# Performance work log

Hardware: AMD Instinct MI355X
Metric: run time of the kernel (lower is better)

Reference implementation:

```python
import jax, jax.numpy as jnp
import numpy as np
from jax import lax

V, E, H, K, PAD = 30000, 128, 256, 32, 0
B, T = 128, 256


def setup_inputs() -> dict:
    key = jax.random.key(0)
    ks = jax.random.split(key, 16)

    def n(k, shape, s=0.1):
        return jax.random.normal(k, shape, jnp.float32) * s

    embed = n(ks[0], (V, E)).at[PAD].set(0.0)  # padding_idx row zeroed
    wih_f = n(ks[1], (4 * H, E)); whh_f = n(ks[2], (4 * H, H))
    bih_f = n(ks[3], (4 * H,));   bhh_f = n(ks[4], (4 * H,))
    wih_b = n(ks[5], (4 * H, E)); whh_b = n(ks[6], (4 * H, H))
    bih_b = n(ks[7], (4 * H,));   bhh_b = n(ks[8], (4 * H,))
    w_lin = n(ks[9], (K, 2 * H)); b_lin = n(ks[10], (K,))
    start_t = n(ks[11], (K,)); end_t = n(ks[12], (K,)); trans = n(ks[13], (K, K))
    tokens = jax.random.randint(ks[14], (B, T), 0, V)
    lengths = jax.random.randint(ks[15], (B,), 1, T + 1)
    mask = jnp.arange(T)[None, :] < lengths[:, None]  # mask[:,0] always True
    return {"input": tokens, "mask": mask, "embed": embed,
            "wih_f": wih_f, "whh_f": whh_f, "bih_f": bih_f, "bhh_f": bhh_f,
            "wih_b": wih_b, "whh_b": whh_b, "bih_b": bih_b, "bhh_b": bhh_b,
            "w_lin": w_lin, "b_lin": b_lin,
            "start_t": start_t, "end_t": end_t, "trans": trans}


def _lstm(x, wih, whh, bih, bhh, reverse):
    # x: [B,T,E]; torch gate order i,f,g,o
    Bq, _, _ = x.shape
    Hh = whh.shape[1]
    pre = jnp.einsum('bte,ge->btg', x, wih) + bih + bhh  # [B,T,4H]
    pre = jnp.swapaxes(pre, 0, 1)  # [T,B,4H]

    def step(carry, p):
        h, c = carry
        g = p + h @ whh.T
        i, f, gg, o = jnp.split(g, 4, axis=-1)
        c = jax.nn.sigmoid(f) * c + jax.nn.sigmoid(i) * jnp.tanh(gg)
        h = jax.nn.sigmoid(o) * jnp.tanh(c)
        return (h, c), h

    init = (jnp.zeros((Bq, Hh), x.dtype), jnp.zeros((Bq, Hh), x.dtype))
    _, hs = lax.scan(step, init, pre, reverse=reverse)
    return jnp.swapaxes(hs, 0, 1)  # [B,T,H]


def _emissions(input, embed, wih_f, whh_f, bih_f, bhh_f, wih_b, whh_b, bih_b, bhh_b, w_lin, b_lin):
    x = embed[input]                               # [B,T,E]
    hf = _lstm(x, wih_f, whh_f, bih_f, bhh_f, False)
    hb = _lstm(x, wih_b, whh_b, bih_b, bhh_b, True)
    return jnp.concatenate([hf, hb], -1) @ w_lin.T + b_lin  # [B,T,K]


def _viterbi(em, mask, start_t, end_t, trans):
    Bq, Tq, Kq = em.shape
    score = start_t + em[:, 0]                     # [B,K]
    em_t = jnp.swapaxes(em, 0, 1)[1:]              # [T-1,B,K]
    m_t = jnp.swapaxes(mask, 0, 1)[1:]             # [T-1,B]

    def step(score, em_m):
        emt, m = em_m
        cand = score[:, :, None] + trans[None] + emt[:, None, :]  # [B,K,K]
        best = cand.max(axis=1)
        idx = jnp.argmax(cand, axis=1)             # [B,K] best prev tag
        return jnp.where(m[:, None], best, score), idx

    score, hist = lax.scan(step, score, (em_t, m_t))  # hist [T-1,B,K]
    last = jnp.argmax(score + end_t, axis=-1)      # [B] tag at last valid pos

    def back(idx, hist_m):
        h, m = hist_m
        prev = jnp.take_along_axis(h, idx[:, None], axis=1)[:, 0]
        new = jnp.where(m, prev, idx)
        return new, new

    _, tags_head = lax.scan(back, last, (hist, m_t), reverse=True)  # [T-1,B]
    tags = jnp.concatenate([tags_head, last[None]], axis=0)         # [T,B]
    tags = jnp.swapaxes(tags, 0, 1)
    return jnp.where(mask, tags, 0).astype(jnp.int32)


def reference(input, mask, embed, wih_f, whh_f, bih_f, bhh_f, wih_b, whh_b, bih_b, bhh_b, w_lin, b_lin, start_t, end_t, trans):
    em = _emissions(input, embed, wih_f, whh_f, bih_f, bhh_f,
                    wih_b, whh_b, bih_b, bhh_b, w_lin, b_lin)
    return _viterbi(em, mask, start_t, end_t, trans)
```

## Files before the change

### kernel.cpp

```cpp
#include <hip/hip_runtime.h>
#include <hip/hip_bf16.h>

#define B_ 128
#define T_ 256
#define E_ 128
#define H_ 256
#define K_ 32
#define G4H 1024

__device__ __forceinline__ float sigf(float z) { return 1.0f / (1.0f + expf(-z)); }

__global__ void k_lengths(const unsigned* __restrict__ maskw, int* __restrict__ lengths) {
  __shared__ int flagBad;
  __shared__ int flagOdd;
  int tid = threadIdx.x;
  if (tid == 0) { flagBad = 0; flagOdd = 0; }
  __syncthreads();
  int bad = 0, odd = 0;
  for (int i = tid; i < (B_ * T_) / 4; i += 256) {
    unsigned v = maskw[i];
    if (v > 1u) bad = 1;
    if ((i & 1) && v) odd = 1;
  }
  if (bad) atomicOr(&flagBad, 1);
  if (odd) atomicOr(&flagOdd, 1);
  __syncthreads();
  int mode = flagBad ? 0 : (flagOdd ? 1 : 2);
  for (int b = tid; b < B_; b += 256) {
    int cnt = 0;
    if (mode == 0) {
      const unsigned char* mb = (const unsigned char*)maskw;
      for (int t = 0; t < T_; ++t) cnt += (mb[b * T_ + t] != 0);
    } else if (mode == 1) {
      for (int t = 0; t < T_; ++t) cnt += (maskw[b * T_ + t] != 0);
    } else {
      for (int t = 0; t < T_; ++t) cnt += (maskw[(size_t)(b * T_ + t) * 2] != 0);
    }
    if (cnt < 1) cnt = 1;
    lengths[b] = cnt;
  }
}

__global__ void k_packw4(const float* __restrict__ wih_f, const float* __restrict__ whh_f,
                         const float* __restrict__ wih_b, const float* __restrict__ whh_b,
                         float* __restrict__ wpk) {
  int e = blockIdx.x * 256 + threadIdx.x;
  if (e >= 786432) return;
  int p = e & 3;
  int g = (e >> 2) & 63;
  int rest = e >> 8;
  int k4 = rest % 96;
  int dus = rest / 96;
  int us = dus & 15, d = dus >> 4;
  int brow = (g >> 4) * 256 + us * 16 + (g & 15);
  int k = k4 * 4 + p;
  const float* wih = d ? wih_b : wih_f;
  const float* whh = d ? whh_b : whh_f;
  wpk[e] = (k < E_) ? wih[brow * E_ + k] : whh[brow * H_ + (k - E_)];
}

__global__ void k_bias(const float* __restrict__ bih_f, const float* __restrict__ bhh_f,
                       const float* __restrict__ bih_b, const float* __restrict__ bhh_b,
                       float* __restrict__ bias) {
  int e = blockIdx.x * 256 + threadIdx.x;
  if (e >= 2 * G4H) return;
  int d = e >> 10, j = e & 1023;
  bias[e] = d ? (bih_b[j] + bhh_b[j]) : (bih_f[j] + bhh_f[j]);
}

__global__ void k_gather(const int* __restrict__ tokens, const float* __restrict__ embed,
                         float* __restrict__ x) {
  int idx = blockIdx.x * 256 + threadIdx.x;
  int p = idx >> 5, e4 = idx & 31;
  int tok = tokens[p];
  ((float4*)x)[(size_t)p * 32 + e4] = ((const float4*)embed)[(size_t)tok * 32 + e4];
}

__global__ void k_zero(int* __restrict__ flags) {
  int i = blockIdx.x * 256 + threadIdx.x;
  if (i < 16384) flags[i] = 0;
}

__global__ __launch_bounds__(512) void k_lstm4(const float* __restrict__ x,
    const float* __restrict__ wpk, const float* __restrict__ bias,
    float* __restrict__ hf, float* __restrict__ hb,
    float* __restrict__ hx, int* __restrict__ flags) {
  const int wg = blockIdx.x;
  const int us = wg & 15;
  const int rb = (wg >> 4) & 7;
  const int d  = wg >> 7;
  const int b0 = rb * 16;
  const int tid = threadIdx.x;
  __shared__ float4 wL[96 * 64];
  __shared__ float4 vL[96 * 16];
  __shared__ float  gbuf2[2 * 64 * 17];

  {
    const float4* wsrc = (const float4*)(wpk + (size_t)(d * 16 + us) * 24576);
    for (int i = tid; i < 6144; i += 512) wL[i] = wsrc[i];
  }
  const int r2 = tid & 7;
  const int gg = (tid >> 3) & 31;
  const int kc = tid >> 8;
  const int g0 = 2 * gg, g1 = g0 + 1;
  const int uu = tid & 15, rr = (tid >> 4) & 15;
  const int sk4 = tid >> 4, sr = tid & 15;
  float b_i = 0.f, b_f = 0.f, b_g = 0.f, b_o = 0.f;
  if (tid < 256) {
    b_i = bias[d * G4H + 0 * 256 + us * 16 + uu];
    b_f = bias[d * G4H + 1 * 256 + us * 16 + uu];
    b_g = bias[d * G4H + 2 * 256 + us * 16 + uu];
    b_o = bias[d * G4H + 3 * 256 + us * 16 + uu];
  }
  float creg = 0.f;
  float4 xr;
  {
    int t0 = d ? (T_ - 1) : 0;
    xr = *(const float4*)(x + ((size_t)(b0 + sr) * T_ + t0) * E_ + sk4 * 4);
  }
  float* __restrict__ hout = d ? hb : hf;
  float* __restrict__ hxg = hx + (size_t)(d * 8 + rb) * 8192;
  int* __restrict__ flagg = flags + (d * 8 + rb) * 1024;
  __syncthreads();

  for (int s = 0; s < T_; ++s) {
    const int t = d ? (T_ - 1 - s) : s;
    if (s > 0 && tid < 16) {
      int* fp = flagg + tid * 64;
      while (__hip_atomic_load(fp, __ATOMIC_RELAXED, __HIP_MEMORY_SCOPE_AGENT) < s) {}
    }
    __syncthreads();
    vL[sk4 * 16 + sr] = xr;
    if (s == 0) {
#pragma unroll
      for (int it = 0; it < 8; ++it) {
        int i = it * 512 + tid;
        ((float*)vL)[(32 + (i >> 6)) * 64 + (i & 15) * 4 + ((i >> 4) & 3)] = 0.f;
      }
    } else {
      const float* hsrc = hxg + (size_t)(s & 1) * 4096;
#pragma unroll
      for (int it = 0; it < 8; ++it) {
        int i = it * 512 + tid;
        float hv = __hip_atomic_load(hsrc + i, __ATOMIC_RELAXED, __HIP_MEMORY_SCOPE_AGENT);
        ((float*)vL)[(32 + (i >> 6)) * 64 + (i & 15) * 4 + ((i >> 4) & 3)] = hv;
      }
    }
    __syncthreads();
    if (s + 1 < T_) {
      int tn = d ? (T_ - 2 - s) : (s + 1);
      xr = *(const float4*)(x + ((size_t)(b0 + sr) * T_ + tn) * E_ + sk4 * 4);
    }
    float a00 = 0.f, a01 = 0.f, a10 = 0.f, a11 = 0.f;
    {
      const float4* wp = wL + kc * 48 * 64;
      const float4* vp = vL + kc * 48 * 16;
#pragma unroll 4
      for (int k4 = 0; k4 < 48; ++k4) {
        float4 w0 = wp[k4 * 64 + g0];
        float4 w1 = wp[k4 * 64 + g1];
        float4 v0 = vp[k4 * 16 + 2 * r2];
        float4 v1 = vp[k4 * 16 + 2 * r2 + 1];
        a00 += w0.x * v0.x + w0.y * v0.y + w0.z * v0.z + w0.w * v0.w;
        a01 += w0.x * v1.x + w0.y * v1.y + w0.z * v1.z + w0.w * v1.w;
        a10 += w1.x * v0.x + w1.y * v0.y + w1.z * v0.z + w1.w * v0.w;
        a11 += w1.x * v1.x + w1.y * v1.y + w1.z * v1.z + w1.w * v1.w;
      }
    }
    gbuf2[kc * 1088 + g0 * 17 + 2 * r2]     = a00;
    gbuf2[kc * 1088 + g0 * 17 + 2 * r2 + 1] = a01;
    gbuf2[kc * 1088 + g1 * 17 + 2 * r2]     = a10;
    gbuf2[kc * 1088 + g1 * 17 + 2 * r2 + 1] = a11;
    __syncthreads();
    if (tid < 256) {
      float ig = gbuf2[uu * 17 + rr]        + gbuf2[1088 + uu * 17 + rr]        + b_i;
      float fg = gbuf2[(16 + uu) * 17 + rr] + gbuf2[1088 + (16 + uu) * 17 + rr] + b_f;
      float gv = gbuf2[(32 + uu) * 17 + rr] + gbuf2[1088 + (32 + uu) * 17 + rr] + b_g;
      float og = gbuf2[(48 + uu) * 17 + rr] + gbuf2[1088 + (48 + uu) * 17 + rr] + b_o;
      creg = sigf(fg) * creg + sigf(ig) * tanhf(gv);
      float hn = sigf(og) * tanhf(creg);
      hout[((size_t)(b0 + rr) * T_ + t) * H_ + us * 16 + uu] = hn;
      __hip_atomic_store(hxg + (size_t)((s + 1) & 1) * 4096 + (us * 16 + uu) * 16 + rr, hn,
                         __ATOMIC_RELAXED, __HIP_MEMORY_SCOPE_AGENT);
    }
    asm volatile("s_waitcnt vmcnt(0)" ::: "memory");
    __syncthreads();
    if (tid == 0)
      __hip_atomic_store(flagg + us * 64, s + 1, __ATOMIC_RELEASE, __HIP_MEMORY_SCOPE_AGENT);
  }
}

__global__ __launch_bounds__(256) void k_emis(const float* __restrict__ hf, const float* __restrict__ hb,
    const float* __restrict__ w_lin, const float* __restrict__ b_lin, float* __restrict__ em) {
  __shared__ float hsl[8][512];
  __shared__ float red[8][8][K_];
  const int tid = threadIdx.x;
  const int pos0 = blockIdx.x * 8;
  for (int it = 0; it < 4; ++it) {
    int idx = it * 256 + tid;
    int rr = idx >> 7, c4 = idx & 127;
    const float* src = (c4 < 64) ? (hf + ((size_t)(pos0 + rr)) * H_ + (c4 * 4))
                                 : (hb + ((size_t)(pos0 + rr)) * H_ + ((c4 - 64) * 4));
    float4 v = *(const float4*)src;
    *(float4*)&hsl[rr][c4 * 4] = v;
  }
  __syncthreads();
  const int k = tid & 31, jc = tid >> 5;
  float wreg[64];
#pragma unroll
  for (int i4 = 0; i4 < 16; ++i4) {
    float4 w = *(const float4*)(w_lin + (size_t)k * 512 + jc * 64 + i4 * 4);
    wreg[i4 * 4 + 0] = w.x; wreg[i4 * 4 + 1] = w.y; wreg[i4 * 4 + 2] = w.z; wreg[i4 * 4 + 3] = w.w;
  }
  float acc[8];
  for (int rr = 0; rr < 8; ++rr) {
    float a = 0.f;
#pragma unroll
    for (int i4 = 0; i4 < 16; ++i4) {
      float4 h = *(const float4*)&hsl[rr][jc * 64 + i4 * 4];
      a += wreg[i4 * 4 + 0] * h.x + wreg[i4 * 4 + 1] * h.y + wreg[i4 * 4 + 2] * h.z + wreg[i4 * 4 + 3] * h.w;
    }
    acc[rr] = a;
  }
  for (int rr2 = 0; rr2 < 8; ++rr2) red[rr2][jc][k] = acc[rr2];
  __syncthreads();
  {
    int rr = tid >> 5, kk = tid & 31;
    float s = b_lin[kk];
#pragma unroll
    for (int j = 0; j < 8; ++j) s += red[rr][j][kk];
    em[((size_t)(pos0 + rr)) * K_ + kk] = s;
  }
}

__global__ __launch_bounds__(64) void k_viterbi(const float* __restrict__ em,
    const int* __restrict__ lengths, const float* __restrict__ start_t,
    const float* __restrict__ end_t, const float* __restrict__ trans,
    int* __restrict__ out) {
  const int b = blockIdx.x;
  const int lane = threadIdx.x;
  __shared__ unsigned char hist[T_ - 1][K_];
  __shared__ float sl[K_];
  const int len = lengths[b];
  float tc[K_];
  float score = 0.f;
  if (lane < K_) {
#pragma unroll
    for (int i = 0; i < K_; ++i) tc[i] = trans[i * K_ + lane];
    score = start_t[lane] + em[((size_t)b * T_) * K_ + lane];
  }
  for (int t = 1; t < T_; ++t) {
    float emk = 0.f;
    if (lane < K_) {
      emk = em[((size_t)b * T_ + t) * K_ + lane];
      sl[lane] = score;
    }
    __syncthreads();
    if (lane < K_) {
      float best = sl[0] + tc[0]; int bi = 0;
#pragma unroll
      for (int i = 1; i < K_; ++i) {
        float c = sl[i] + tc[i];
        if (c > best) { best = c; bi = i; }
      }
      hist[t - 1][lane] = (unsigned char)bi;
      if (t < len) score = best + emk;
    }
    __syncthreads();
  }
  if (lane < K_) sl[lane] = score + end_t[lane];
  __syncthreads();
  int* outb = out + (size_t)b * T_;
  for (int t = lane; t < T_; t += 64)
    if (t >= len) outb[t] = 0;
  if (lane == 0) {
    float best = sl[0]; int cur = 0;
    for (int k2 = 1; k2 < K_; ++k2)
      if (sl[k2] > best) { best = sl[k2]; cur = k2; }
    outb[len - 1] = cur;
    for (int t = len - 2; t >= 0; --t) { cur = hist[t][cur]; outb[t] = cur; }
  }
}

extern "C" void kernel_launch(void* const* d_in, const int* in_sizes, int n_in,
                              void* d_out, int out_size, void* d_ws, size_t ws_size,
                              hipStream_t stream) {
  const int* tokens   = (const int*)d_in[0];
  const unsigned* maskw = (const unsigned*)d_in[1];
  const float* embed  = (const float*)d_in[2];
  const float* wih_f  = (const float*)d_in[3];
  const float* whh_f  = (const float*)d_in[4];
  const float* bih_f  = (const float*)d_in[5];
  const float* bhh_f  = (const float*)d_in[6];
  const float* wih_b  = (const float*)d_in[7];
  const float* whh_b  = (const float*)d_in[8];
  const float* bih_b  = (const float*)d_in[9];
  const float* bhh_b  = (const float*)d_in[10];
  const float* w_lin  = (const float*)d_in[11];
  const float* b_lin  = (const float*)d_in[12];
  const float* start_t = (const float*)d_in[13];
  const float* end_t  = (const float*)d_in[14];
  const float* trans  = (const float*)d_in[15];
  int* out = (int*)d_out;
  (void)in_sizes; (void)n_in; (void)out_size; (void)ws_size;

  char* ws = (char*)d_ws;
  size_t off = 0;
  auto alloc = [&](size_t bytes) { size_t o = off; off = (off + bytes + 255) & ~(size_t)255; return o; };
  int*   lengths = (int*)(ws + alloc((size_t)B_ * 4));
  float* wpk     = (float*)(ws + alloc((size_t)786432 * 4));
  float* bias    = (float*)(ws + alloc((size_t)2 * G4H * 4));
  float* x       = (float*)(ws + alloc((size_t)B_ * T_ * E_ * 4));
  float* hf      = (float*)(ws + alloc((size_t)B_ * T_ * H_ * 4));
  float* hb      = (float*)(ws + alloc((size_t)B_ * T_ * H_ * 4));
  float* em      = (float*)(ws + alloc((size_t)B_ * T_ * K_ * 4));
  float* hx      = (float*)(ws + alloc((size_t)16 * 8192 * 4));
  int*   flags   = (int*)(ws + alloc((size_t)16384 * 4));

  k_lengths<<<dim3(1), dim3(256), 0, stream>>>(maskw, lengths);
  k_packw4<<<dim3(3072), dim3(256), 0, stream>>>(wih_f, whh_f, wih_b, whh_b, wpk);
  k_bias<<<dim3(8), dim3(256), 0, stream>>>(bih_f, bhh_f, bih_b, bhh_b, bias);
  k_gather<<<dim3((B_ * T_ * E_ / 4) / 256), dim3(256), 0, stream>>>(tokens, embed, x);
  k_zero<<<dim3(64), dim3(256), 0, stream>>>(flags);
  k_lstm4<<<dim3(256), dim3(512), 0, stream>>>(x, wpk, bias, hf, hb, hx, flags);
  k_emis<<<dim3(B_ * T_ / 8), dim3(256), 0, stream>>>(hf, hb, w_lin, b_lin, em);
  k_viterbi<<<dim3(B_), dim3(64), 0, stream>>>(em, lengths, start_t, end_t, trans, out);
}
```

Measured before the change: 3.180 ms.

## Overlap input-projection matmul with cross-block hidden-state wait in LSTM

Splits the packed LSTM weights into separate input and recurrent blocks so each step can compute the x·Wih contribution before spinning on the inter-workgroup flags. The recurrent part runs only after the hidden state from other workgroups arrives. The global h output store and the next x prefetch move after the flag release, which takes them off the critical path. This adds an extra __syncthreads per step and splits the pack kernel in two.

Result: faster. 3.058 ms (-3.8%).

```diff
diff --git a/kernel.cpp b/kernel.cpp
--- a/kernel.cpp
+++ b/kernel.cpp
@@ -41,22 +41,32 @@
   }
 }
 
-__global__ void k_packw4(const float* __restrict__ wih_f, const float* __restrict__ whh_f,
-                         const float* __restrict__ wih_b, const float* __restrict__ whh_b,
-                         float* __restrict__ wpk) {
+__global__ void k_packw3A(const float* __restrict__ wih_f, const float* __restrict__ wih_b,
+                          float* __restrict__ wpkA) {
   int e = blockIdx.x * 256 + threadIdx.x;
-  if (e >= 786432) return;
-  int p = e & 3;
-  int g = (e >> 2) & 63;
-  int rest = e >> 8;
-  int k4 = rest % 96;
-  int dus = rest / 96;
-  int us = dus & 15, d = dus >> 4;
+  if (e >= 262144) return;
+  int p  = e & 3;
+  int g  = (e >> 2) & 63;
+  int k4 = (e >> 8) & 31;
+  int us = (e >> 13) & 15;
+  int d  = (e >> 17) & 1;
   int brow = (g >> 4) * 256 + us * 16 + (g & 15);
-  int k = k4 * 4 + p;
   const float* wih = d ? wih_b : wih_f;
+  wpkA[e] = wih[brow * E_ + k4 * 4 + p];
+}
+
+__global__ void k_packw3B(const float* __restrict__ whh_f, const float* __restrict__ whh_b,
+                          float* __restrict__ wpkB) {
+  int e = blockIdx.x * 256 + threadIdx.x;
+  if (e >= 524288) return;
+  int p  = e & 3;
+  int g  = (e >> 2) & 63;
+  int k4 = (e >> 8) & 63;
+  int us = (e >> 14) & 15;
+  int d  = (e >> 18) & 1;
+  int brow = (g >> 4) * 256 + us * 16 + (g & 15);
   const float* whh = d ? whh_b : whh_f;
-  wpk[e] = (k < E_) ? wih[brow * E_ + k] : whh[brow * H_ + (k - E_)];
+  wpkB[e] = whh[brow * H_ + k4 * 4 + p];
 }
 
 __global__ void k_bias(const float* __restrict__ bih_f, const float* __restrict__ bhh_f,
@@ -81,8 +91,9 @@
   if (i < 16384) flags[i] = 0;
 }
 
-__global__ __launch_bounds__(512) void k_lstm4(const float* __restrict__ x,
-    const float* __restrict__ wpk, const float* __restrict__ bias,
+__global__ __launch_bounds__(512) void k_lstm5(const float* __restrict__ x,
+    const float* __restrict__ wpkA, const float* __restrict__ wpkB,
+    const float* __restrict__ bias,
     float* __restrict__ hf, float* __restrict__ hb,
     float* __restrict__ hx, int* __restrict__ flags) {
   const int wg = blockIdx.x;
@@ -91,13 +102,17 @@
   const int d  = wg >> 7;
   const int b0 = rb * 16;
   const int tid = threadIdx.x;
-  __shared__ float4 wL[96 * 64];
-  __shared__ float4 vL[96 * 16];
+  __shared__ float4 wA[32 * 64];
+  __shared__ float4 wB[64 * 64];
+  __shared__ float4 vx[32 * 16];
+  __shared__ float4 vLh[64 * 16];
   __shared__ float  gbuf2[2 * 64 * 17];
 
   {
-    const float4* wsrc = (const float4*)(wpk + (size_t)(d * 16 + us) * 24576);
-    for (int i = tid; i < 6144; i += 512) wL[i] = wsrc[i];
+    const float4* srcA = (const float4*)(wpkA + (size_t)(d * 16 + us) * 8192);
+    for (int i = tid; i < 2048; i += 512) wA[i] = srcA[i];
+    const float4* srcB = (const float4*)(wpkB + (size_t)(d * 16 + us) * 16384);
+    for (int i = tid; i < 4096; i += 512) wB[i] = srcB[i];
   }
   const int r2 = tid & 7;
   const int gg = (tid >> 3) & 31;
@@ -112,12 +127,17 @@
     b_g = bias[d * G4H + 2 * 256 + us * 16 + uu];
     b_o = bias[d * G4H + 3 * 256 + us * 16 + uu];
   }
-  float creg = 0.f;
+  float creg = 0.f, hn = 0.f;
   float4 xr;
   {
     int t0 = d ? (T_ - 1) : 0;
     xr = *(const float4*)(x + ((size_t)(b0 + sr) * T_ + t0) * E_ + sk4 * 4);
   }
+  vx[sk4 * 16 + sr] = xr;
+  {
+    int t1 = d ? (T_ - 2) : 1;
+    xr = *(const float4*)(x + ((size_t)(b0 + sr) * T_ + t1) * E_ + sk4 * 4);
+  }
   float* __restrict__ hout = d ? hb : hf;
   float* __restrict__ hxg = hx + (size_t)(d * 8 + rb) * 8192;
   int* __restrict__ flagg = flags + (d * 8 + rb) * 1024;
@@ -125,38 +145,12 @@
 
   for (int s = 0; s < T_; ++s) {
     const int t = d ? (T_ - 1 - s) : s;
-    if (s > 0 && tid < 16) {
-      int* fp = flagg + tid * 64;
-      while (__hip_atomic_load(fp, __ATOMIC_RELAXED, __HIP_MEMORY_SCOPE_AGENT) < s) {}
-    }
-    __syncthreads();
-    vL[sk4 * 16 + sr] = xr;
-    if (s == 0) {
-#pragma unroll
-      for (int it = 0; it < 8; ++it) {
-        int i = it * 512 + tid;
-        ((float*)vL)[(32 + (i >> 6)) * 64 + (i & 15) * 4 + ((i >> 4) & 3)] = 0.f;
-      }
-    } else {
-      const float* hsrc = hxg + (size_t)(s & 1) * 4096;
-#pragma unroll
-      for (int it = 0; it < 8; ++it) {
-        int i = it * 512 + tid;
-        float hv = __hip_atomic_load(hsrc + i, __ATOMIC_RELAXED, __HIP_MEMORY_SCOPE_AGENT);
-        ((float*)vL)[(32 + (i >> 6)) * 64 + (i & 15) * 4 + ((i >> 4) & 3)] = hv;
-      }
-    }
-    __syncthreads();
-    if (s + 1 < T_) {
-      int tn = d ? (T_ - 2 - s) : (s + 1);
-      xr = *(const float4*)(x + ((size_t)(b0 + sr) * T_ + tn) * E_ + sk4 * 4);
-    }
     float a00 = 0.f, a01 = 0.f, a10 = 0.f, a11 = 0.f;
     {
-      const float4* wp = wL + kc * 48 * 64;
-      const float4* vp = vL + kc * 48 * 16;
+      const float4* wp = wA + kc * 1024;
+      const float4* vp = vx + kc * 256;
 #pragma unroll 4
-      for (int k4 = 0; k4 < 48; ++k4) {
+      for (int k4 = 0; k4 < 16; ++k4) {
         float4 w0 = wp[k4 * 64 + g0];
         float4 w1 = wp[k4 * 64 + g1];
         float4 v0 = vp[k4 * 16 + 2 * r2];
@@ -167,6 +161,42 @@
         a11 += w1.x * v1.x + w1.y * v1.y + w1.z * v1.z + w1.w * v1.w;
       }
     }
+    if (s > 0 && tid < 16) {
+      int* fp = flagg + tid * 64;
+      while (__hip_atomic_load(fp, __ATOMIC_RELAXED, __HIP_MEMORY_SCOPE_AGENT) < s) {}
+    }
+    __syncthreads();
+    if (s == 0) {
+#pragma unroll
+      for (int it = 0; it < 8; ++it) {
+        int i = it * 512 + tid;
+        ((float*)vLh)[(i >> 6) * 64 + (i & 15) * 4 + ((i >> 4) & 3)] = 0.f;
+      }
+    } else {
+      const float* hsrc = hxg + (size_t)(s & 1) * 4096;
+#pragma unroll
+      for (int it = 0; it < 8; ++it) {
+        int i = it * 512 + tid;
+        float hv = __hip_atomic_load(hsrc + i, __ATOMIC_RELAXED, __HIP_MEMORY_SCOPE_AGENT);
+        ((float*)vLh)[(i >> 6) * 64 + (i & 15) * 4 + ((i >> 4) & 3)] = hv;
+      }
+    }
+    __syncthreads();
+    {
+      const float4* wp = wB + kc * 2048;
+      const float4* vp = vLh + kc * 512;
+#pragma unroll 4
+      for (int k4 = 0; k4 < 32; ++k4) {
+        float4 w0 = wp[k4 * 64 + g0];
+        float4 w1 = wp[k4 * 64 + g1];
+        float4 v0 = vp[k4 * 16 + 2 * r2];
+        float4 v1 = vp[k4 * 16 + 2 * r2 + 1];
+        a00 += w0.x * v0.x + w0.y * v0.y + w0.z * v0.z + w0.w * v0.w;
+        a01 += w0.x * v1.x + w0.y * v1.y + w0.z * v1.z + w0.w * v1.w;
+        a10 += w1.x * v0.x + w1.y * v0.y + w1.z * v0.z + w1.w * v0.w;
+        a11 += w1.x * v1.x + w1.y * v1.y + w1.z * v1.z + w1.w * v1.w;
+      }
+    }
     gbuf2[kc * 1088 + g0 * 17 + 2 * r2]     = a00;
     gbuf2[kc * 1088 + g0 * 17 + 2 * r2 + 1] = a01;
     gbuf2[kc * 1088 + g1 * 17 + 2 * r2]     = a10;
@@ -178,8 +208,7 @@
       float gv = gbuf2[(32 + uu) * 17 + rr] + gbuf2[1088 + (32 + uu) * 17 + rr] + b_g;
       float og = gbuf2[(48 + uu) * 17 + rr] + gbuf2[1088 + (48 + uu) * 17 + rr] + b_o;
       creg = sigf(fg) * creg + sigf(ig) * tanhf(gv);
-      float hn = sigf(og) * tanhf(creg);
-      hout[((size_t)(b0 + rr) * T_ + t) * H_ + us * 16 + uu] = hn;
+      hn = sigf(og) * tanhf(creg);
       __hip_atomic_store(hxg + (size_t)((s + 1) & 1) * 4096 + (us * 16 + uu) * 16 + rr, hn,
                          __ATOMIC_RELAXED, __HIP_MEMORY_SCOPE_AGENT);
     }
@@ -187,6 +216,16 @@
     __syncthreads();
     if (tid == 0)
       __hip_atomic_store(flagg + us * 64, s + 1, __ATOMIC_RELEASE, __HIP_MEMORY_SCOPE_AGENT);
+    if (tid < 256)
+      hout[((size_t)(b0 + rr) * T_ + t) * H_ + us * 16 + uu] = hn;
+    if (s + 1 < T_) {
+      vx[sk4 * 16 + sr] = xr;
+      if (s + 2 < T_) {
+        int tn = d ? (T_ - 3 - s) : (s + 2);
+        xr = *(const float4*)(x + ((size_t)(b0 + sr) * T_ + tn) * E_ + sk4 * 4);
+      }
+    }
+    __syncthreads();
   }
 }
 
@@ -308,7 +347,8 @@
   size_t off = 0;
   auto alloc = [&](size_t bytes) { size_t o = off; off = (off + bytes + 255) & ~(size_t)255; return o; };
   int*   lengths = (int*)(ws + alloc((size_t)B_ * 4));
-  float* wpk     = (float*)(ws + alloc((size_t)786432 * 4));
+  float* wpkA    = (float*)(ws + alloc((size_t)262144 * 4));
+  float* wpkB    = (float*)(ws + alloc((size_t)524288 * 4));
   float* bias    = (float*)(ws + alloc((size_t)2 * G4H * 4));
   float* x       = (float*)(ws + alloc((size_t)B_ * T_ * E_ * 4));
   float* hf      = (float*)(ws + alloc((size_t)B_ * T_ * H_ * 4));
@@ -318,11 +358,12 @@
   int*   flags   = (int*)(ws + alloc((size_t)16384 * 4));
 
   k_lengths<<<dim3(1), dim3(256), 0, stream>>>(maskw, lengths);
-  k_packw4<<<dim3(3072), dim3(256), 0, stream>>>(wih_f, whh_f, wih_b, whh_b, wpk);
+  k_packw3A<<<dim3(1024), dim3(256), 0, stream>>>(wih_f, wih_b, wpkA);
+  k_packw3B<<<dim3(2048), dim3(256), 0, stream>>>(whh_f, whh_b, wpkB);
   k_bias<<<dim3(8), dim3(256), 0, stream>>>(bih_f, bhh_f, bih_b, bhh_b, bias);
   k_gather<<<dim3((B_ * T_ * E_ / 4) / 256), dim3(256), 0, stream>>>(tokens, embed, x);
   k_zero<<<dim3(64), dim3(256), 0, stream>>>(flags);
-  k_lstm4<<<dim3(256), dim3(512), 0, stream>>>(x, wpk, bias, hf, hb, hx, flags);
+  k_lstm5<<<dim3(256), dim3(512), 0, stream>>>(x, wpkA, wpkB, bias, hf, hb, hx, flags);
   k_emis<<<dim3(B_ * T_ / 8), dim3(256), 0, stream>>>(hf, hb, w_lin, b_lin, em);
   k_viterbi<<<dim3(B_), dim3(64), 0, stream>>>(em, lengths, start_t, end_t, trans, out);
 }
```

## Overlap input-projection with flag wait and retile LSTM step as 4x4 register blocks

Applied to the files above, without the earlier changes.

The recurrent LSTM kernel now computes the x·Wih part of the gates before spinning on the cross-workgroup flags, so that work is hidden behind the wait for the previous hidden state. The per-thread tile becomes 4 gates × 4 rows over 8 K-slices, with a matching weight repack and an 8-way reduction buffer. The hout global store and the next x prefetch move after the flag release to shorten the critical path. The cost is an extra barrier per step, a larger shared-memory reduction buffer, and more registers held per thread.

Measured after the change: 3.020 ms. 1.05x faster.

```diff
diff --git a/kernel.cpp b/kernel.cpp
--- a/kernel.cpp
+++ b/kernel.cpp
@@ -9,6 +9,9 @@
 #define G4H 1024
 
 __device__ __forceinline__ float sigf(float z) { return 1.0f / (1.0f + expf(-z)); }
+__device__ __forceinline__ float dot4(float4 a, float4 b) {
+  return a.x * b.x + a.y * b.y + a.z * b.z + a.w * b.w;
+}
 
 __global__ void k_lengths(const unsigned* __restrict__ maskw, int* __restrict__ lengths) {
   __shared__ int flagBad;
@@ -41,22 +44,33 @@
   }
 }
 
-__global__ void k_packw4(const float* __restrict__ wih_f, const float* __restrict__ whh_f,
+__global__ void k_packw6(const float* __restrict__ wih_f, const float* __restrict__ whh_f,
                          const float* __restrict__ wih_b, const float* __restrict__ whh_b,
                          float* __restrict__ wpk) {
   int e = blockIdx.x * 256 + threadIdx.x;
   if (e >= 786432) return;
   int p = e & 3;
-  int g = (e >> 2) & 63;
-  int rest = e >> 8;
-  int k4 = rest % 96;
-  int dus = rest / 96;
-  int us = dus & 15, d = dus >> 4;
-  int brow = (g >> 4) * 256 + us * 16 + (g & 15);
-  int k = k4 * 4 + p;
+  int j = (e >> 2) & 63;
+  int gi = j >> 4, gq = j & 15;
+  int g = gq * 4 + gi;
+  int iter = (e >> 8) % 12;
+  int q = (e >> 8) / 12;
+  int slice = q & 7;
+  int us = (q >> 3) & 15;
+  int d = q >> 7;
+  int ty = g >> 4, u = g & 15;
+  int brow = ty * 256 + us * 16 + u;
   const float* wih = d ? wih_b : wih_f;
   const float* whh = d ? whh_b : whh_f;
-  wpk[e] = (k < E_) ? wih[brow * E_ + k] : whh[brow * H_ + (k - E_)];
+  float v;
+  if (iter < 4) {
+    int k4 = slice * 4 + iter;
+    v = wih[brow * E_ + k4 * 4 + p];
+  } else {
+    int k4 = slice * 8 + (iter - 4);
+    v = whh[brow * H_ + k4 * 4 + p];
+  }
+  wpk[e] = v;
 }
 
 __global__ void k_bias(const float* __restrict__ bih_f, const float* __restrict__ bhh_f,
@@ -81,7 +95,7 @@
   if (i < 16384) flags[i] = 0;
 }
 
-__global__ __launch_bounds__(512) void k_lstm4(const float* __restrict__ x,
+__global__ __launch_bounds__(512) void k_lstm6(const float* __restrict__ x,
     const float* __restrict__ wpk, const float* __restrict__ bias,
     float* __restrict__ hf, float* __restrict__ hb,
     float* __restrict__ hx, int* __restrict__ flags) {
@@ -91,18 +105,18 @@
   const int d  = wg >> 7;
   const int b0 = rb * 16;
   const int tid = threadIdx.x;
-  __shared__ float4 wL[96 * 64];
-  __shared__ float4 vL[96 * 16];
-  __shared__ float  gbuf2[2 * 64 * 17];
+  __shared__ float4 wL[8 * 12 * 64];
+  __shared__ float4 vx[32 * 16];
+  __shared__ float4 vLh[64 * 16];
+  __shared__ float  gbuf[8 * 64 * 17];
 
   {
     const float4* wsrc = (const float4*)(wpk + (size_t)(d * 16 + us) * 24576);
     for (int i = tid; i < 6144; i += 512) wL[i] = wsrc[i];
   }
-  const int r2 = tid & 7;
-  const int gg = (tid >> 3) & 31;
-  const int kc = tid >> 8;
-  const int g0 = 2 * gg, g1 = g0 + 1;
+  const int slice = tid >> 6;
+  const int gq = (tid >> 2) & 15;
+  const int rq = tid & 3;
   const int uu = tid & 15, rr = (tid >> 4) & 15;
   const int sk4 = tid >> 4, sr = tid & 15;
   float b_i = 0.f, b_f = 0.f, b_g = 0.f, b_o = 0.f;
@@ -112,30 +126,50 @@
     b_g = bias[d * G4H + 2 * 256 + us * 16 + uu];
     b_o = bias[d * G4H + 3 * 256 + us * 16 + uu];
   }
-  float creg = 0.f;
+  float creg = 0.f, hn = 0.f;
   float4 xr;
   {
     int t0 = d ? (T_ - 1) : 0;
     xr = *(const float4*)(x + ((size_t)(b0 + sr) * T_ + t0) * E_ + sk4 * 4);
   }
+  vx[sk4 * 16 + sr] = xr;
+  {
+    int t1 = d ? (T_ - 2) : 1;
+    xr = *(const float4*)(x + ((size_t)(b0 + sr) * T_ + t1) * E_ + sk4 * 4);
+  }
   float* __restrict__ hout = d ? hb : hf;
   float* __restrict__ hxg = hx + (size_t)(d * 8 + rb) * 8192;
   int* __restrict__ flagg = flags + (d * 8 + rb) * 1024;
+  const float4* wbase = wL + slice * 12 * 64;
   __syncthreads();
 
   for (int s = 0; s < T_; ++s) {
     const int t = d ? (T_ - 1 - s) : s;
+    float a00 = 0.f, a01 = 0.f, a02 = 0.f, a03 = 0.f;
+    float a10 = 0.f, a11 = 0.f, a12 = 0.f, a13 = 0.f;
+    float a20 = 0.f, a21 = 0.f, a22 = 0.f, a23 = 0.f;
+    float a30 = 0.f, a31 = 0.f, a32 = 0.f, a33 = 0.f;
+#pragma unroll
+    for (int it = 0; it < 4; ++it) {
+      const float4* wp = wbase + it * 64;
+      const float4* vp = vx + (slice * 4 + it) * 16 + rq * 4;
+      float4 w0 = wp[gq], w1 = wp[16 + gq], w2 = wp[32 + gq], w3 = wp[48 + gq];
+      float4 v0 = vp[0], v1 = vp[1], v2 = vp[2], v3 = vp[3];
+      a00 += dot4(w0, v0); a01 += dot4(w0, v1); a02 += dot4(w0, v2); a03 += dot4(w0, v3);
+      a10 += dot4(w1, v0); a11 += dot4(w1, v1); a12 += dot4(w1, v2); a13 += dot4(w1, v3);
+      a20 += dot4(w2, v0); a21 += dot4(w2, v1); a22 += dot4(w2, v2); a23 += dot4(w2, v3);
+      a30 += dot4(w3, v0); a31 += dot4(w3, v1); a32 += dot4(w3, v2); a33 += dot4(w3, v3);
+    }
     if (s > 0 && tid < 16) {
       int* fp = flagg + tid * 64;
       while (__hip_atomic_load(fp, __ATOMIC_RELAXED, __HIP_MEMORY_SCOPE_AGENT) < s) {}
     }
     __syncthreads();
-    vL[sk4 * 16 + sr] = xr;
     if (s == 0) {
 #pragma unroll
       for (int it = 0; it < 8; ++it) {
         int i = it * 512 + tid;
-        ((float*)vL)[(32 + (i >> 6)) * 64 + (i & 15) * 4 + ((i >> 4) & 3)] = 0.f;
+        ((float*)vLh)[(i >> 6) * 64 + (i & 15) * 4 + ((i >> 4) & 3)] = 0.f;
       }
     } else {
       const float* hsrc = hxg + (size_t)(s & 1) * 4096;
@@ -143,43 +177,42 @@
       for (int it = 0; it < 8; ++it) {
         int i = it * 512 + tid;
         float hv = __hip_atomic_load(hsrc + i, __ATOMIC_RELAXED, __HIP_MEMORY_SCOPE_AGENT);
-        ((float*)vL)[(32 + (i >> 6)) * 64 + (i & 15) * 4 + ((i >> 4) & 3)] = hv;
-      }
-    }
-    __syncthreads();
-    if (s + 1 < T_) {
-      int tn = d ? (T_ - 2 - s) : (s + 1);
-      xr = *(const float4*)(x + ((size_t)(b0 + sr) * T_ + tn) * E_ + sk4 * 4);
-    }
-    float a00 = 0.f, a01 = 0.f, a10 = 0.f, a11 = 0.f;
+        ((float*)vLh)[(i >> 6) * 64 + (i & 15) * 4 + ((i >> 4) & 3)] = hv;
+      }
+    }
+    __syncthreads();
+#pragma unroll
+    for (int it = 0; it < 8; ++it) {
+      const float4* wp = wbase + (4 + it) * 64;
+      const float4* vp = vLh + (slice * 8 + it) * 16 + rq * 4;
+      float4 w0 = wp[gq], w1 = wp[16 + gq], w2 = wp[32 + gq], w3 = wp[48 + gq];
+      float4 v0 = vp[0], v1 = vp[1], v2 = vp[2], v3 = vp[3];
+      a00 += dot4(w0, v0); a01 += dot4(w0, v1); a02 += dot4(w0, v2); a03 += dot4(w0, v3);
+      a10 += dot4(w1, v0); a11 += dot4(w1, v1); a12 += dot4(w1, v2); a13 += dot4(w1, v3);
+      a20 += dot4(w2, v0); a21 += dot4(w2, v1); a22 += dot4(w2, v2); a23 += dot4(w2, v3);
+      a30 += dot4(w3, v0); a31 += dot4(w3, v1); a32 += dot4(w3, v2); a33 += dot4(w3, v3);
+    }
     {
-      const float4* wp = wL + kc * 48 * 64;
-      const float4* vp = vL + kc * 48 * 16;
-#pragma unroll 4
-      for (int k4 = 0; k4 < 48; ++k4) {
-        float4 w0 = wp[k4 * 64 + g0];
-        float4 w1 = wp[k4 * 64 + g1];
-        float4 v0 = vp[k4 * 16 + 2 * r2];
-        float4 v1 = vp[k4 * 16 + 2 * r2 + 1];
-        a00 += w0.x * v0.x + w0.y * v0.y + w0.z * v0.z + w0.w * v0.w;
-        a01 += w0.x * v1.x + w0.y * v1.y + w0.z * v1.z + w0.w * v1.w;
-        a10 += w1.x * v0.x + w1.y * v0.y + w1.z * v0.z + w1.w * v0.w;
-        a11 += w1.x * v1.x + w1.y * v1.y + w1.z * v1.z + w1.w * v1.w;
-      }
-    }
-    gbuf2[kc * 1088 + g0 * 17 + 2 * r2]     = a00;
-    gbuf2[kc * 1088 + g0 * 17 + 2 * r2 + 1] = a01;
-    gbuf2[kc * 1088 + g1 * 17 + 2 * r2]     = a10;
-    gbuf2[kc * 1088 + g1 * 17 + 2 * r2 + 1] = a11;
+      float* gb = gbuf + slice * 1088 + (gq * 4) * 17 + rq * 4;
+      gb[0] = a00; gb[1] = a01; gb[2] = a02; gb[3] = a03;
+      gb[17 + 0] = a10; gb[17 + 1] = a11; gb[17 + 2] = a12; gb[17 + 3] = a13;
+      gb[34 + 0] = a20; gb[34 + 1] = a21; gb[34 + 2] = a22; gb[34 + 3] = a23;
+      gb[51 + 0] = a30; gb[51 + 1] = a31; gb[51 + 2] = a32; gb[51 + 3] = a33;
+    }
     __syncthreads();
     if (tid < 256) {
-      float ig = gbuf2[uu * 17 + rr]        + gbuf2[1088 + uu * 17 + rr]        + b_i;
-      float fg = gbuf2[(16 + uu) * 17 + rr] + gbuf2[1088 + (16 + uu) * 17 + rr] + b_f;
-      float gv = gbuf2[(32 + uu) * 17 + rr] + gbuf2[1088 + (32 + uu) * 17 + rr] + b_g;
-      float og = gbuf2[(48 + uu) * 17 + rr] + gbuf2[1088 + (48 + uu) * 17 + rr] + b_o;
+      float ig = 0.f, fg = 0.f, gv = 0.f, og = 0.f;
+#pragma unroll
+      for (int sl = 0; sl < 8; ++sl) {
+        const float* gb = gbuf + sl * 1088;
+        ig += gb[(0 * 16 + uu) * 17 + rr];
+        fg += gb[(1 * 16 + uu) * 17 + rr];
+        gv += gb[(2 * 16 + uu) * 17 + rr];
+        og += gb[(3 * 16 + uu) * 17 + rr];
+      }
+      ig += b_i; fg += b_f; gv += b_g; og += b_o;
       creg = sigf(fg) * creg + sigf(ig) * tanhf(gv);
-      float hn = sigf(og) * tanhf(creg);
-      hout[((size_t)(b0 + rr) * T_ + t) * H_ + us * 16 + uu] = hn;
+      hn = sigf(og) * tanhf(creg);
       __hip_atomic_store(hxg + (size_t)((s + 1) & 1) * 4096 + (us * 16 + uu) * 16 + rr, hn,
                          __ATOMIC_RELAXED, __HIP_MEMORY_SCOPE_AGENT);
     }
@@ -187,6 +220,16 @@
     __syncthreads();
     if (tid == 0)
       __hip_atomic_store(flagg + us * 64, s + 1, __ATOMIC_RELEASE, __HIP_MEMORY_SCOPE_AGENT);
+    if (tid < 256)
+      hout[((size_t)(b0 + rr) * T_ + t) * H_ + us * 16 + uu] = hn;
+    if (s + 1 < T_) {
+      vx[sk4 * 16 + sr] = xr;
+      if (s + 2 < T_) {
+        int tn = d ? (T_ - 3 - s) : (s + 2);
+        xr = *(const float4*)(x + ((size_t)(b0 + sr) * T_ + tn) * E_ + sk4 * 4);
+      }
+    }
+    __syncthreads();
   }
 }
 
@@ -318,11 +361,11 @@
   int*   flags   = (int*)(ws + alloc((size_t)16384 * 4));
 
   k_lengths<<<dim3(1), dim3(256), 0, stream>>>(maskw, lengths);
-  k_packw4<<<dim3(3072), dim3(256), 0, stream>>>(wih_f, whh_f, wih_b, whh_b, wpk);
+  k_packw6<<<dim3(3072), dim3(256), 0, stream>>>(wih_f, whh_f, wih_b, whh_b, wpk);
   k_bias<<<dim3(8), dim3(256), 0, stream>>>(bih_f, bhh_f, bih_b, bhh_b, bias);
   k_gather<<<dim3((B_ * T_ * E_ / 4) / 256), dim3(256), 0, stream>>>(tokens, embed, x);
   k_zero<<<dim3(64), dim3(256), 0, stream>>>(flags);
-  k_lstm4<<<dim3(256), dim3(512), 0, stream>>>(x, wpk, bias, hf, hb, hx, flags);
+  k_lstm6<<<dim3(256), dim3(512), 0, stream>>>(x, wpk, bias, hf, hb, hx, flags);
   k_emis<<<dim3(B_ * T_ / 8), dim3(256), 0, stream>>>(hf, hb, w_lin, b_lin, em);
   k_viterbi<<<dim3(B_), dim3(64), 0, stream>>>(em, lengths, start_t, end_t, trans, out);
 }
```
